# Kernel tuning notes

Hardware: AMD Instinct MI355X
Metric: run time of the kernel (lower is better)

The kernel has to match this reference:

```python
import jax, jax.numpy as jnp
import numpy as np

LN_EPS = 1e-5


def _segment_mean(vals, idx, num_segments):
    s = jax.ops.segment_sum(vals, idx, num_segments=num_segments)
    cnt = jax.ops.segment_sum(jnp.ones((vals.shape[0],), vals.dtype), idx, num_segments=num_segments)
    return s / jnp.maximum(cnt, 1.0)[:, None]


def _sage_layer(x, src, dst, W_l, b_l, W_r, gamma, beta):
    # PyG SAGEConv (mean aggr): out = lin_l(mean_{j in N(i)} x_j) + lin_r(x_i)
    N = x.shape[0]
    agg = _segment_mean(x[src], dst, N)                     # [N, in]
    h = agg @ W_l.T + b_l + x @ W_r.T                       # [N, out]
    mu = jnp.mean(h, axis=-1, keepdims=True)
    var = jnp.mean((h - mu) ** 2, axis=-1, keepdims=True)
    h = (h - mu) * jax.lax.rsqrt(var + LN_EPS) * gamma + beta
    return jax.nn.relu(h)                                   # dropout: eval mode (identity)


def setup_inputs() -> dict:
    key = jax.random.key(0)
    ks = jax.random.split(key, 20)
    N, E, IN, H, OUT, G, C = 50000, 600000, 128, 128, 64, 64, 2

    def glorot(k, fo, fi):
        lim = np.sqrt(6.0 / (fo + fi)).astype(np.float32)
        return jax.random.uniform(k, (fo, fi), jnp.float32, -lim, lim)

    inp = {
        'x': jax.random.normal(ks[0], (N, IN), jnp.float32),
        'edge_index': jax.random.randint(ks[1], (2, E), 0, N, jnp.int64),
        'batch': jnp.sort(jax.random.randint(ks[2], (N,), 0, G, jnp.int64)),
    }
    dims = [(IN, H), (H, H), (H, OUT)]
    for i, (fi, fo) in enumerate(dims):
        inp[f'Wl{i}'] = glorot(ks[3 + 4 * i], fo, fi)
        inp[f'bl{i}'] = jnp.zeros((fo,), jnp.float32)
        inp[f'Wr{i}'] = glorot(ks[4 + 4 * i], fo, fi)
        inp[f'g{i}'] = jnp.ones((fo,), jnp.float32)
        inp[f'be{i}'] = jnp.zeros((fo,), jnp.float32)
    inp['cW1'] = glorot(ks[16], H, 2 * OUT)
    inp['cb1'] = jnp.zeros((H,), jnp.float32)
    inp['cW2'] = glorot(ks[17], C, H)
    inp['cb2'] = jnp.zeros((C,), jnp.float32)
    return inp


def reference(x, edge_index, batch,
              Wl0, bl0, Wr0, g0, be0,
              Wl1, bl1, Wr1, g1, be1,
              Wl2, bl2, Wr2, g2, be2,
              cW1, cb1, cW2, cb2):
    src, dst = edge_index[0], edge_index[1]
    h = _sage_layer(x, src, dst, Wl0, bl0, Wr0, g0, be0)
    h = _sage_layer(h, src, dst, Wl1, bl1, Wr1, g1, be1)
    h = _sage_layer(h, src, dst, Wl2, bl2, Wr2, g2, be2)
    G = 64  # number of graphs
    x_mean = _segment_mean(h, batch, G)                     # [G, out]
    x_max = jax.ops.segment_max(h, batch, num_segments=G)   # [G, out]
    z = jnp.concatenate([x_mean, x_max], axis=-1)           # [G, 2*out]
    z = jax.nn.relu(z @ cW1.T + cb1)
    return z @ cW2.T + cb2                                  # [G, num_classes]
```

## Files before the change

kernel.cpp:

```cpp
#include <hip/hip_runtime.h>

typedef unsigned short ushort_t;
typedef short s16x8 __attribute__((ext_vector_type(8)));
typedef float f32x4 __attribute__((ext_vector_type(4)));

#define LN_EPS 1e-5f

__device__ __forceinline__ float b2f(ushort_t u) {
    return __uint_as_float(((unsigned)u) << 16);
}
__device__ __forceinline__ ushort_t f2b(float f) {
    unsigned b = __float_as_uint(f);
    b += 0x7FFFu + ((b >> 16) & 1u);
    return (ushort_t)(b >> 16);
}
__device__ __forceinline__ float ldf(const void* p, size_t i, int isF) {
    return isF ? ((const float*)p)[i] : b2f(((const ushort_t*)p)[i]);
}

__global__ void GraphSAGE_36026185678961_kernel() {}

__global__ void k_detect(const void* w0, const void* ei, int* __restrict__ flags) {
    int t = threadIdx.x;
    const ushort_t* u = (const ushort_t*)w0;
    int pass = 0;
    #pragma unroll
    for (int k = 0; k < 4; ++k) {
        ushort_t v = u[t * 4 + k];
        int ex = (v >> 7) & 0xFF;
        if (ex == 0 || (ex >= 0x60 && ex <= 0x7E)) pass++;
    }
    const unsigned* w = (const unsigned*)ei;
    int nz = (w[2 * t + 1] != 0u) ? 1 : 0;
    #pragma unroll
    for (int off = 32; off; off >>= 1) {
        pass += __shfl_down(pass, off, 64);
        nz += __shfl_down(nz, off, 64);
    }
    if (t == 0) {
        flags[0] = (pass < 205) ? 1 : 0;
        flags[1] = (nz == 0) ? 1 : 0;
    }
}

__global__ void k_zero(int* __restrict__ deg, float* __restrict__ Z, int N) {
    int i = blockIdx.x * blockDim.x + threadIdx.x;
    if (i < N) deg[i] = 0;
    if (i < 64 * 128) Z[i] = 0.f;
}

__global__ void k_xconv(const void* X, const int* __restrict__ flags,
                        ushort_t* __restrict__ XB, int total4) {
    int idx = blockIdx.x * blockDim.x + threadIdx.x;
    if (idx >= total4) return;
    if (flags[0]) {
        float4 v = ((const float4*)X)[idx];
        ushort4 o;
        o.x = f2b(v.x); o.y = f2b(v.y); o.z = f2b(v.z); o.w = f2b(v.w);
        ((ushort4*)XB)[idx] = o;
    } else {
        ((ushort4*)XB)[idx] = ((const ushort4*)X)[idx];
    }
}

__global__ void k_edges(const void* ei, int E, const int* __restrict__ flags,
                        int* __restrict__ s32, int* __restrict__ d32) {
    int e = blockIdx.x * blockDim.x + threadIdx.x;
    if (e >= E) return;
    if (flags[1]) {
        const long long* p = (const long long*)ei;
        s32[e] = (int)p[e];
        d32[e] = (int)p[E + e];
    } else {
        const int* p = (const int*)ei;
        s32[e] = p[e];
        d32[e] = p[E + e];
    }
}

__global__ void k_hist(const int* __restrict__ dst, int E, int N, int* __restrict__ deg) {
    int e = blockIdx.x * blockDim.x + threadIdx.x;
    if (e < E) {
        int d = dst[e];
        if ((unsigned)d < (unsigned)N) atomicAdd(&deg[d], 1);
    }
}

__global__ void k_scan1(const int* __restrict__ deg, int N,
                        int* __restrict__ rowptr, int* __restrict__ bsum) {
    __shared__ int wsum[4];
    __shared__ int wpre[4];
    int tid = threadIdx.x;
    int lane = tid & 63;
    int w = tid >> 6;
    int i = blockIdx.x * 256 + tid;
    int v = (i < N) ? deg[i] : 0;
    int x = v;
    #pragma unroll
    for (int off = 1; off < 64; off <<= 1) {
        int t = __shfl_up(x, off, 64);
        if (lane >= off) x += t;
    }
    if (lane == 63) wsum[w] = x;
    __syncthreads();
    if (tid == 0) {
        int a = wsum[0]; wpre[0] = a;
        a += wsum[1]; wpre[1] = a;
        a += wsum[2]; wpre[2] = a;
        a += wsum[3]; wpre[3] = a;
    }
    __syncthreads();
    int woff = (w == 0) ? 0 : wpre[w - 1];
    if (i < N) rowptr[i] = woff + x - v;
    if (tid == 0) bsum[blockIdx.x] = wpre[3];
}

__global__ void k_scan2(const int* __restrict__ bsum, int nb,
                        int* __restrict__ boff, int* __restrict__ rowptrN) {
    __shared__ int wsum[4];
    __shared__ int wpre[4];
    int tid = threadIdx.x;
    int lane = tid & 63;
    int w = tid >> 6;
    int run = 0;
    for (int base = 0; base < nb; base += 256) {
        int i = base + tid;
        int v = (i < nb) ? bsum[i] : 0;
        int x = v;
        #pragma unroll
        for (int off = 1; off < 64; off <<= 1) {
            int t = __shfl_up(x, off, 64);
            if (lane >= off) x += t;
        }
        if (lane == 63) wsum[w] = x;
        __syncthreads();
        if (tid == 0) {
            int a = wsum[0]; wpre[0] = a;
            a += wsum[1]; wpre[1] = a;
            a += wsum[2]; wpre[2] = a;
            a += wsum[3]; wpre[3] = a;
        }
        __syncthreads();
        int woff = (w == 0) ? 0 : wpre[w - 1];
        if (i < nb) boff[i] = run + woff + x - v;
        int tot = wpre[3];
        __syncthreads();
        run += tot;
    }
    if (tid == 0) *rowptrN = run;
}

__global__ void k_scan3(int* __restrict__ rowptr, const int* __restrict__ boff,
                        int* __restrict__ cursor, int N) {
    int i = blockIdx.x * 256 + threadIdx.x;
    if (i < N) {
        int r = rowptr[i] + boff[i >> 8];
        rowptr[i] = r;
        cursor[i] = r;
    }
}

__global__ void k_fill(const int* __restrict__ src, const int* __restrict__ dst, int E, int N,
                       int* __restrict__ cursor, int* __restrict__ col) {
    int e = blockIdx.x * blockDim.x + threadIdx.x;
    if (e < E) {
        int d = dst[e];
        if ((unsigned)d < (unsigned)N) {
            int p = atomicAdd(&cursor[d], 1);
            if ((unsigned)p < (unsigned)E) {
                int s = src[e];
                col[p] = ((unsigned)s < (unsigned)N) ? s : 0;
            }
        }
    }
}

__global__ void k_bounds(const void* batch, int N, int G, const int* __restrict__ flags,
                         int* __restrict__ bounds) {
    int g = threadIdx.x;
    if (g > G) return;
    int isL = flags[1];
    int lo = 0, hi = N;
    while (lo < hi) {
        int mid = (lo + hi) >> 1;
        int bv = isL ? (int)((const long long*)batch)[mid] : ((const int*)batch)[mid];
        if (bv < g) lo = mid + 1; else hi = mid;
    }
    bounds[g] = lo;
}

__global__ __launch_bounds__(256) void k_agg(
    const ushort_t* __restrict__ X, const int* __restrict__ rowptr,
    const int* __restrict__ col, ushort_t* __restrict__ AGG, int N) {
    int i = blockIdx.x * 4 + (threadIdx.x >> 6);
    if (i >= N) return;
    int l = threadIdx.x & 63;
    const ushort2* X2 = (const ushort2*)X;
    int s = rowptr[i], e = rowptr[i + 1];
    float a0 = 0.f, b0 = 0.f, a1 = 0.f, b1 = 0.f;
    int p = s;
    for (; p + 4 <= e; p += 4) {
        int j0 = col[p], j1 = col[p + 1], j2 = col[p + 2], j3 = col[p + 3];
        ushort2 u0 = X2[(size_t)j0 * 64 + l];
        ushort2 u1 = X2[(size_t)j1 * 64 + l];
        ushort2 u2 = X2[(size_t)j2 * 64 + l];
        ushort2 u3 = X2[(size_t)j3 * 64 + l];
        a0 += b2f(u0.x); b0 += b2f(u0.y);
        a1 += b2f(u1.x); b1 += b2f(u1.y);
        a0 += b2f(u2.x); b0 += b2f(u2.y);
        a1 += b2f(u3.x); b1 += b2f(u3.y);
    }
    for (; p < e; ++p) {
        int j = col[p];
        ushort2 u = X2[(size_t)j * 64 + l];
        a0 += b2f(u.x); b0 += b2f(u.y);
    }
    int d = e - s;
    float inv = 1.f / (float)(d > 0 ? d : 1);
    ushort2 o;
    o.x = f2b((a0 + a1) * inv);
    o.y = f2b((b0 + b1) * inv);
    ((ushort2*)AGG)[(size_t)i * 64 + l] = o;
}

template <int FO>
__global__ void k_wprep(const void* Wl, const void* Wr, const int* __restrict__ flags,
                        ushort_t* __restrict__ Wb) {
    int t = blockIdx.x * blockDim.x + threadIdx.x;
    if (t >= 256 * FO) return;
    int isF = flags[0];
    int f = t >> 8, k = t & 255;
    float v = (k < 128) ? ldf(Wl, f * 128 + k, isF) : ldf(Wr, f * 128 + (k - 128), isF);
    Wb[t] = isF ? f2b(v) : ((const ushort_t*)((k < 128) ? Wl : Wr))[f * 128 + (k & 127)];
}

template <int FO>
__global__ __launch_bounds__(256) void k_gemm_ln(
    const ushort_t* __restrict__ AGG, const ushort_t* __restrict__ X,
    const ushort_t* __restrict__ Wb,
    const void* bl, const void* gam, const void* bet,
    const int* __restrict__ flags,
    ushort_t* __restrict__ H, int M) {
    constexpr int NT = FO / 16;
    int lane = threadIdx.x & 63;
    int wid = threadIdx.x >> 6;
    int row0 = (blockIdx.x * 4 + wid) * 16;
    if (row0 >= M) return;
    int isF = flags[0];
    int m = lane & 15;
    int q = lane >> 4;

    int arow = row0 + m;
    if (arow >= M) arow = M - 1;
    const ushort_t* aA = AGG + (size_t)arow * 128 + q * 8;
    const ushort_t* aX = X + (size_t)arow * 128 + q * 8;
    const ushort_t* bW = Wb + (size_t)m * 256 + q * 8;

    f32x4 acc[NT];
    #pragma unroll
    for (int nt = 0; nt < NT; ++nt) acc[nt] = (f32x4){0.f, 0.f, 0.f, 0.f};

    #pragma unroll
    for (int kk = 0; kk < 4; ++kk) {
        s16x8 a = *(const s16x8*)(aA + kk * 32);
        #pragma unroll
        for (int nt = 0; nt < NT; ++nt) {
            s16x8 b = *(const s16x8*)(bW + (size_t)nt * 16 * 256 + kk * 32);
            acc[nt] = __builtin_amdgcn_mfma_f32_16x16x32_bf16(a, b, acc[nt], 0, 0, 0);
        }
    }
    #pragma unroll
    for (int kk = 0; kk < 4; ++kk) {
        s16x8 a = *(const s16x8*)(aX + kk * 32);
        #pragma unroll
        for (int nt = 0; nt < NT; ++nt) {
            s16x8 b = *(const s16x8*)(bW + (size_t)nt * 16 * 256 + 128 + kk * 32);
            acc[nt] = __builtin_amdgcn_mfma_f32_16x16x32_bf16(a, b, acc[nt], 0, 0, 0);
        }
    }

    #pragma unroll
    for (int nt = 0; nt < NT; ++nt) {
        float bv = ldf(bl, nt * 16 + m, isF);
        #pragma unroll
        for (int r = 0; r < 4; ++r) acc[nt][r] += bv;
    }

    float mu[4], rs[4];
    #pragma unroll
    for (int r = 0; r < 4; ++r) {
        float s1 = 0.f, s2 = 0.f;
        #pragma unroll
        for (int nt = 0; nt < NT; ++nt) {
            float v = acc[nt][r];
            s1 += v;
            s2 += v * v;
        }
        #pragma unroll
        for (int off = 1; off < 16; off <<= 1) {
            s1 += __shfl_xor(s1, off, 64);
            s2 += __shfl_xor(s2, off, 64);
        }
        float mm = s1 / (float)FO;
        float var = s2 / (float)FO - mm * mm;
        var = var > 0.f ? var : 0.f;
        mu[r] = mm;
        rs[r] = rsqrtf(var + LN_EPS);
    }

    #pragma unroll
    for (int nt = 0; nt < NT; ++nt) {
        int n0 = nt * 16 + m;
        float g = ldf(gam, n0, isF);
        float be = ldf(bet, n0, isF);
        #pragma unroll
        for (int r = 0; r < 4; ++r) {
            int row = row0 + q * 4 + r;
            if (row < M) {
                float y = (acc[nt][r] - mu[r]) * rs[r] * g + be;
                y = y > 0.f ? y : 0.f;
                H[(size_t)row * FO + n0] = f2b(y);
            }
        }
    }
}

__global__ void k_pool(const ushort_t* __restrict__ H,
                       const int* __restrict__ bounds, float* __restrict__ Z, int N) {
    int g = blockIdx.x >> 3;
    int chunk = blockIdx.x & 7;
    int f = threadIdx.x & 63;
    int sub = threadIdx.x >> 6;
    int strm = chunk * 4 + sub;
    int s = bounds[g], e = bounds[g + 1];
    s = s < 0 ? 0 : (s > N ? N : s);
    e = e < s ? s : (e > N ? N : e);
    float sum = 0.f, mx = 0.f;
    for (int i = s + strm; i < e; i += 32) {
        float v = b2f(H[(size_t)i * 64 + f]);
        sum += v;
        mx = mx > v ? mx : v;
    }
    atomicAdd(&Z[g * 128 + f], sum);
    atomicMax((int*)&Z[g * 128 + 64 + f], __float_as_int(mx));
}

__global__ void k_mlp(const float* __restrict__ Z, const int* __restrict__ bounds,
                      const void* cW1, const void* cb1, const void* cW2, const void* cb2,
                      const int* __restrict__ flags, void* __restrict__ out) {
    int g = blockIdx.x;
    int f = threadIdx.x;
    int isF = flags[0];
    __shared__ float z[128];
    __shared__ float hid[128];
    __shared__ float r0[2], r1[2];
    int cnt = bounds[g + 1] - bounds[g];
    float c = (float)(cnt > 0 ? cnt : 1);
    float zv = Z[g * 128 + f];
    if (f < 64) zv /= c;
    z[f] = zv;
    __syncthreads();
    float acc = ldf(cb1, f, isF);
    #pragma unroll 8
    for (int k = 0; k < 128; ++k) acc += z[k] * ldf(cW1, f * 128 + k, isF);
    acc = acc > 0.f ? acc : 0.f;
    hid[f] = acc;
    __syncthreads();
    float p0 = hid[f] * ldf(cW2, f, isF);
    float p1 = hid[f] * ldf(cW2, 128 + f, isF);
    #pragma unroll
    for (int off = 32; off > 0; off >>= 1) {
        p0 += __shfl_xor(p0, off, 64);
        p1 += __shfl_xor(p1, off, 64);
    }
    int w = f >> 6;
    if ((f & 63) == 0) { r0[w] = p0; r1[w] = p1; }
    __syncthreads();
    if (f == 0) {
        float v0 = r0[0] + r0[1] + ldf(cb2, 0, isF);
        float v1 = r1[0] + r1[1] + ldf(cb2, 1, isF);
        if (isF) {
            ((float*)out)[g * 2 + 0] = v0;
            ((float*)out)[g * 2 + 1] = v1;
        } else {
            ((ushort_t*)out)[g * 2 + 0] = f2b(v0);
            ((ushort_t*)out)[g * 2 + 1] = f2b(v1);
        }
    }
}

extern "C" void kernel_launch(void* const* d_in, const int* in_sizes, int n_in,
                              void* d_out, int out_size, void* d_ws, size_t ws_size,
                              hipStream_t stream) {
    const void* x = d_in[0];
    const void* ei = d_in[1];
    const void* batch = d_in[2];
    const void* Wl0 = d_in[3];
    const void* bl0 = d_in[4];
    const void* Wr0 = d_in[5];
    const void* g0 = d_in[6];
    const void* be0 = d_in[7];
    const void* Wl1 = d_in[8];
    const void* bl1 = d_in[9];
    const void* Wr1 = d_in[10];
    const void* g1 = d_in[11];
    const void* be1 = d_in[12];
    const void* Wl2 = d_in[13];
    const void* bl2 = d_in[14];
    const void* Wr2 = d_in[15];
    const void* g2 = d_in[16];
    const void* be2 = d_in[17];
    const void* cW1 = d_in[18];
    const void* cb1 = d_in[19];
    const void* cW2 = d_in[20];
    const void* cb2 = d_in[21];

    const int N = in_sizes[0] / 128;
    const int E = in_sizes[1] / 2;
    const int G = 64;

    char* w = (char*)d_ws;
    size_t o = 0;
    auto take = [&](size_t bytes) -> void* {
        void* p = w + o;
        o = (o + bytes + 255) & ~(size_t)255;
        return p;
    };
    int nb1 = (N + 255) / 256;
    int* flags  = (int*)take(4 * 4);
    int* rowptr = (int*)take((size_t)(N + 1) * 4);
    int* cursor = (int*)take((size_t)N * 4);
    int* deg    = (int*)take((size_t)N * 4);
    int* bsum   = (int*)take((size_t)nb1 * 4);
    int* boff   = (int*)take((size_t)nb1 * 4);
    int* col    = (int*)take((size_t)E * 4);
    int* src32  = (int*)take((size_t)E * 4);
    int* dst32  = (int*)take((size_t)E * 4);
    int* bounds = (int*)take((size_t)(G + 1) * 4);
    float* Z    = (float*)take((size_t)G * 128 * 4);
    ushort_t* Wb0 = (ushort_t*)take((size_t)128 * 256 * 2);
    ushort_t* Wb1 = (ushort_t*)take((size_t)128 * 256 * 2);
    ushort_t* Wb2 = (ushort_t*)take((size_t)64 * 256 * 2);
    ushort_t* AGG = (ushort_t*)take((size_t)N * 128 * 2);
    ushort_t* H1  = (ushort_t*)take((size_t)N * 128 * 2);
    ushort_t* H2  = (ushort_t*)take((size_t)N * 128 * 2);
    ushort_t* XB  = H2;
    ushort_t* H3  = H1;
    if (o > ws_size) return;

    int eb = (E + 255) / 256;
    k_detect<<<1, 64, 0, stream>>>(Wl0, ei, flags);
    k_zero<<<nb1, 256, 0, stream>>>(deg, Z, N);
    k_xconv<<<(N * 128 / 4 + 255) / 256, 256, 0, stream>>>(x, flags, XB, N * 128 / 4);
    k_edges<<<eb, 256, 0, stream>>>(ei, E, flags, src32, dst32);
    k_hist<<<eb, 256, 0, stream>>>(dst32, E, N, deg);
    k_scan1<<<nb1, 256, 0, stream>>>(deg, N, rowptr, bsum);
    k_scan2<<<1, 256, 0, stream>>>(bsum, nb1, boff, rowptr + N);
    k_scan3<<<nb1, 256, 0, stream>>>(rowptr, boff, cursor, N);
    k_fill<<<eb, 256, 0, stream>>>(src32, dst32, E, N, cursor, col);
    k_bounds<<<1, 128, 0, stream>>>(batch, N, G, flags, bounds);
    k_wprep<128><<<128, 256, 0, stream>>>(Wl0, Wr0, flags, Wb0);
    k_wprep<128><<<128, 256, 0, stream>>>(Wl1, Wr1, flags, Wb1);
    k_wprep<64><<<64, 256, 0, stream>>>(Wl2, Wr2, flags, Wb2);

    int gb = (N + 63) / 64;
    int ab = (N + 3) / 4;

    k_agg<<<ab, 256, 0, stream>>>(XB, rowptr, col, AGG, N);
    k_gemm_ln<128><<<gb, 256, 0, stream>>>(AGG, XB, Wb0, bl0, g0, be0, flags, H1, N);
    k_agg<<<ab, 256, 0, stream>>>(H1, rowptr, col, AGG, N);
    k_gemm_ln<128><<<gb, 256, 0, stream>>>(AGG, H1, Wb1, bl1, g1, be1, flags, H2, N);
    k_agg<<<ab, 256, 0, stream>>>(H2, rowptr, col, AGG, N);
    k_gemm_ln<64><<<gb, 256, 0, stream>>>(AGG, H2, Wb2, bl2, g2, be2, flags, H3, N);

    k_pool<<<G * 8, 256, 0, stream>>>(H3, bounds, Z, N);
    k_mlp<<<G, 128, 0, stream>>>(Z, bounds, cW1, cb1, cW2, cb2, flags, d_out);
}
```

Measured before the change: 407.3 us.

## Fuse edge histogram, widen aggregation loads, and tile GEMM over more rows

Three separate changes. The degree histogram is folded into the edge conversion kernel, which removes one launch and one reread of the destination array. The aggregation kernel now loads 8-byte ushort4 values, with each half-wave handling alternate neighbors and a final shuffle combining the two halves. The GEMM+LayerNorm kernel has each wave process 64 rows instead of 16, reusing each weight fragment across four MFMA row tiles; in exchange it uses more registers, launches fewer blocks, and is marked launch_bounds(256,1).

```diff
diff --git a/kernel.cpp b/kernel.cpp
--- a/kernel.cpp
+++ b/kernel.cpp
@@ -63,27 +63,23 @@
     }
 }
 
-__global__ void k_edges(const void* ei, int E, const int* __restrict__ flags,
-                        int* __restrict__ s32, int* __restrict__ d32) {
+__global__ void k_edges(const void* ei, int E, int N, const int* __restrict__ flags,
+                        int* __restrict__ s32, int* __restrict__ d32, int* __restrict__ deg) {
     int e = blockIdx.x * blockDim.x + threadIdx.x;
     if (e >= E) return;
+    int s, d;
     if (flags[1]) {
         const long long* p = (const long long*)ei;
-        s32[e] = (int)p[e];
-        d32[e] = (int)p[E + e];
+        s = (int)p[e];
+        d = (int)p[E + e];
     } else {
         const int* p = (const int*)ei;
-        s32[e] = p[e];
-        d32[e] = p[E + e];
-    }
-}
-
-__global__ void k_hist(const int* __restrict__ dst, int E, int N, int* __restrict__ deg) {
-    int e = blockIdx.x * blockDim.x + threadIdx.x;
-    if (e < E) {
-        int d = dst[e];
-        if ((unsigned)d < (unsigned)N) atomicAdd(&deg[d], 1);
-    }
+        s = p[e];
+        d = p[E + e];
+    }
+    s32[e] = s;
+    d32[e] = d;
+    if ((unsigned)d < (unsigned)N) atomicAdd(&deg[d], 1);
 }
 
 __global__ void k_scan1(const int* __restrict__ deg, int N,
@@ -195,32 +191,40 @@
     int i = blockIdx.x * 4 + (threadIdx.x >> 6);
     if (i >= N) return;
     int l = threadIdx.x & 63;
-    const ushort2* X2 = (const ushort2*)X;
+    int half = l >> 5;
+    int fq = l & 31;
+    const ushort4* X4 = (const ushort4*)X;
     int s = rowptr[i], e = rowptr[i + 1];
-    float a0 = 0.f, b0 = 0.f, a1 = 0.f, b1 = 0.f;
-    int p = s;
-    for (; p + 4 <= e; p += 4) {
-        int j0 = col[p], j1 = col[p + 1], j2 = col[p + 2], j3 = col[p + 3];
-        ushort2 u0 = X2[(size_t)j0 * 64 + l];
-        ushort2 u1 = X2[(size_t)j1 * 64 + l];
-        ushort2 u2 = X2[(size_t)j2 * 64 + l];
-        ushort2 u3 = X2[(size_t)j3 * 64 + l];
-        a0 += b2f(u0.x); b0 += b2f(u0.y);
-        a1 += b2f(u1.x); b1 += b2f(u1.y);
-        a0 += b2f(u2.x); b0 += b2f(u2.y);
-        a1 += b2f(u3.x); b1 += b2f(u3.y);
-    }
-    for (; p < e; ++p) {
+    float a0 = 0.f, a1 = 0.f, a2 = 0.f, a3 = 0.f;
+    int p = s + half;
+    for (; p + 2 < e; p += 4) {
+        int j0 = col[p], j1 = col[p + 2];
+        ushort4 u0 = X4[(size_t)j0 * 32 + fq];
+        ushort4 u1 = X4[(size_t)j1 * 32 + fq];
+        a0 += b2f(u0.x) + b2f(u1.x);
+        a1 += b2f(u0.y) + b2f(u1.y);
+        a2 += b2f(u0.z) + b2f(u1.z);
+        a3 += b2f(u0.w) + b2f(u1.w);
+    }
+    for (; p < e; p += 2) {
         int j = col[p];
-        ushort2 u = X2[(size_t)j * 64 + l];
-        a0 += b2f(u.x); b0 += b2f(u.y);
-    }
-    int d = e - s;
-    float inv = 1.f / (float)(d > 0 ? d : 1);
-    ushort2 o;
-    o.x = f2b((a0 + a1) * inv);
-    o.y = f2b((b0 + b1) * inv);
-    ((ushort2*)AGG)[(size_t)i * 64 + l] = o;
+        ushort4 u = X4[(size_t)j * 32 + fq];
+        a0 += b2f(u.x); a1 += b2f(u.y); a2 += b2f(u.z); a3 += b2f(u.w);
+    }
+    a0 += __shfl_xor(a0, 32, 64);
+    a1 += __shfl_xor(a1, 32, 64);
+    a2 += __shfl_xor(a2, 32, 64);
+    a3 += __shfl_xor(a3, 32, 64);
+    if (half == 0) {
+        int d = e - s;
+        float inv = 1.f / (float)(d > 0 ? d : 1);
+        ushort4 o;
+        o.x = f2b(a0 * inv);
+        o.y = f2b(a1 * inv);
+        o.z = f2b(a2 * inv);
+        o.w = f2b(a3 * inv);
+        ((ushort4*)AGG)[(size_t)i * 32 + fq] = o;
+    }
 }
 
 template <int FO>
@@ -235,91 +239,94 @@
 }
 
 template <int FO>
-__global__ __launch_bounds__(256) void k_gemm_ln(
+__global__ __launch_bounds__(256, 1) void k_gemm_ln(
     const ushort_t* __restrict__ AGG, const ushort_t* __restrict__ X,
     const ushort_t* __restrict__ Wb,
     const void* bl, const void* gam, const void* bet,
     const int* __restrict__ flags,
     ushort_t* __restrict__ H, int M) {
     constexpr int NT = FO / 16;
+    constexpr int R = 4;
     int lane = threadIdx.x & 63;
     int wid = threadIdx.x >> 6;
-    int row0 = (blockIdx.x * 4 + wid) * 16;
-    if (row0 >= M) return;
+    int wrow0 = (blockIdx.x * 4 + wid) * (R * 16);
+    if (wrow0 >= M) return;
     int isF = flags[0];
     int m = lane & 15;
     int q = lane >> 4;
 
-    int arow = row0 + m;
-    if (arow >= M) arow = M - 1;
-    const ushort_t* aA = AGG + (size_t)arow * 128 + q * 8;
-    const ushort_t* aX = X + (size_t)arow * 128 + q * 8;
-    const ushort_t* bW = Wb + (size_t)m * 256 + q * 8;
-
-    f32x4 acc[NT];
-    #pragma unroll
-    for (int nt = 0; nt < NT; ++nt) acc[nt] = (f32x4){0.f, 0.f, 0.f, 0.f};
-
-    #pragma unroll
-    for (int kk = 0; kk < 4; ++kk) {
-        s16x8 a = *(const s16x8*)(aA + kk * 32);
+    int arow[R];
+    #pragma unroll
+    for (int r = 0; r < R; ++r) {
+        int ar = wrow0 + r * 16 + m;
+        arow[r] = (ar < M) ? ar : (M - 1);
+    }
+
+    f32x4 acc[R][NT];
+    #pragma unroll
+    for (int r = 0; r < R; ++r)
+        #pragma unroll
+        for (int nt = 0; nt < NT; ++nt) acc[r][nt] = (f32x4){0.f, 0.f, 0.f, 0.f};
+
+    #pragma unroll
+    for (int kk = 0; kk < 8; ++kk) {
+        const ushort_t* base = (kk < 4) ? AGG : X;
+        int ko = (kk & 3) * 32 + q * 8;
+        s16x8 a[R];
+        #pragma unroll
+        for (int r = 0; r < R; ++r)
+            a[r] = *(const s16x8*)(base + (size_t)arow[r] * 128 + ko);
         #pragma unroll
         for (int nt = 0; nt < NT; ++nt) {
-            s16x8 b = *(const s16x8*)(bW + (size_t)nt * 16 * 256 + kk * 32);
-            acc[nt] = __builtin_amdgcn_mfma_f32_16x16x32_bf16(a, b, acc[nt], 0, 0, 0);
-        }
-    }
-    #pragma unroll
-    for (int kk = 0; kk < 4; ++kk) {
-        s16x8 a = *(const s16x8*)(aX + kk * 32);
+            s16x8 b = *(const s16x8*)(Wb + (size_t)(nt * 16 + m) * 256 + kk * 32 + q * 8);
+            #pragma unroll
+            for (int r = 0; r < R; ++r)
+                acc[r][nt] = __builtin_amdgcn_mfma_f32_16x16x32_bf16(a[r], b, acc[r][nt], 0, 0, 0);
+        }
+    }
+
+    #pragma unroll
+    for (int r = 0; r < R; ++r) {
         #pragma unroll
         for (int nt = 0; nt < NT; ++nt) {
-            s16x8 b = *(const s16x8*)(bW + (size_t)nt * 16 * 256 + 128 + kk * 32);
-            acc[nt] = __builtin_amdgcn_mfma_f32_16x16x32_bf16(a, b, acc[nt], 0, 0, 0);
-        }
-    }
-
-    #pragma unroll
-    for (int nt = 0; nt < NT; ++nt) {
-        float bv = ldf(bl, nt * 16 + m, isF);
-        #pragma unroll
-        for (int r = 0; r < 4; ++r) acc[nt][r] += bv;
-    }
-
-    float mu[4], rs[4];
-    #pragma unroll
-    for (int r = 0; r < 4; ++r) {
-        float s1 = 0.f, s2 = 0.f;
+            float bv = ldf(bl, nt * 16 + m, isF);
+            #pragma unroll
+            for (int rr = 0; rr < 4; ++rr) acc[r][nt][rr] += bv;
+        }
+        float mu[4], rs[4];
+        #pragma unroll
+        for (int rr = 0; rr < 4; ++rr) {
+            float s1 = 0.f, s2 = 0.f;
+            #pragma unroll
+            for (int nt = 0; nt < NT; ++nt) {
+                float v = acc[r][nt][rr];
+                s1 += v;
+                s2 += v * v;
+            }
+            #pragma unroll
+            for (int off = 1; off < 16; off <<= 1) {
+                s1 += __shfl_xor(s1, off, 64);
+                s2 += __shfl_xor(s2, off, 64);
+            }
+            float mm = s1 / (float)FO;
+            float var = s2 / (float)FO - mm * mm;
+            var = var > 0.f ? var : 0.f;
+            mu[rr] = mm;
+            rs[rr] = rsqrtf(var + LN_EPS);
+        }
         #pragma unroll
         for (int nt = 0; nt < NT; ++nt) {
-            float v = acc[nt][r];
-            s1 += v;
-            s2 += v * v;
-        }
-        #pragma unroll
-        for (int off = 1; off < 16; off <<= 1) {
-            s1 += __shfl_xor(s1, off, 64);
-            s2 += __shfl_xor(s2, off, 64);
-        }
-        float mm = s1 / (float)FO;
-        float var = s2 / (float)FO - mm * mm;
-        var = var > 0.f ? var : 0.f;
-        mu[r] = mm;
-        rs[r] = rsqrtf(var + LN_EPS);
-    }
-
-    #pragma unroll
-    for (int nt = 0; nt < NT; ++nt) {
-        int n0 = nt * 16 + m;
-        float g = ldf(gam, n0, isF);
-        float be = ldf(bet, n0, isF);
-        #pragma unroll
-        for (int r = 0; r < 4; ++r) {
-            int row = row0 + q * 4 + r;
-            if (row < M) {
-                float y = (acc[nt][r] - mu[r]) * rs[r] * g + be;
-                y = y > 0.f ? y : 0.f;
-                H[(size_t)row * FO + n0] = f2b(y);
+            int n0 = nt * 16 + m;
+            float g = ldf(gam, n0, isF);
+            float be = ldf(bet, n0, isF);
+            #pragma unroll
+            for (int rr = 0; rr < 4; ++rr) {
+                int row = wrow0 + r * 16 + q * 4 + rr;
+                if (row < M) {
+                    float y = (acc[r][nt][rr] - mu[rr]) * rs[rr] * g + be;
+                    y = y > 0.f ? y : 0.f;
+                    H[(size_t)row * FO + n0] = f2b(y);
+                }
             }
         }
     }
@@ -452,8 +459,7 @@
     k_detect<<<1, 64, 0, stream>>>(Wl0, ei, flags);
     k_zero<<<nb1, 256, 0, stream>>>(deg, Z, N);
     k_xconv<<<(N * 128 / 4 + 255) / 256, 256, 0, stream>>>(x, flags, XB, N * 128 / 4);
-    k_edges<<<eb, 256, 0, stream>>>(ei, E, flags, src32, dst32);
-    k_hist<<<eb, 256, 0, stream>>>(dst32, E, N, deg);
+    k_edges<<<eb, 256, 0, stream>>>(ei, E, N, flags, src32, dst32, deg);
     k_scan1<<<nb1, 256, 0, stream>>>(deg, N, rowptr, bsum);
     k_scan2<<<1, 256, 0, stream>>>(bsum, nb1, boff, rowptr + N);
     k_scan3<<<nb1, 256, 0, stream>>>(rowptr, boff, cursor, N);
@@ -463,7 +469,7 @@
     k_wprep<128><<<128, 256, 0, stream>>>(Wl1, Wr1, flags, Wb1);
     k_wprep<64><<<64, 256, 0, stream>>>(Wl2, Wr2, flags, Wb2);
 
-    int gb = (N + 63) / 64;
+    int gb = (N + 255) / 256;
     int ab = (N + 3) / 4;
 
     k_agg<<<ab, 256, 0, stream>>>(XB, rowptr, col, AGG, N);
```

Measured after the change: 393.1 us. 1.04x faster.
